# Performance work log

Hardware: AMD Instinct MI355X
Metric: run time of the kernel (lower is better)

## Reference

```python
import jax, jax.numpy as jnp
import numpy as np

LN_EPS = 1e-5


def setup_inputs() -> dict:
    key = jax.random.key(0)
    k1, k2, k3, k4 = jax.random.split(key, 4)
    b, n, d, o, m = 64, 196, 768, 196, 2
    return {
        "x": jax.random.normal(k1, (b, n, d), dtype=jnp.float32),
        "ln_w": jnp.ones((d,), dtype=jnp.float32),
        "ln_b": jnp.zeros((d,), dtype=jnp.float32),
        "sw": jax.random.normal(k2, (o, m, n), dtype=jnp.float32),
        "sb": jax.random.normal(k3, (o, m, n), dtype=jnp.float32),
        "dw": jax.random.normal(k4, (o, m), dtype=jnp.float32),
    }


def reference(x, ln_w, ln_b, sw, sb, dw):
    # LayerNorm over last dim (dim=768)
    mu = jnp.mean(x, axis=-1, keepdims=True)
    var = jnp.mean(jnp.square(x - mu), axis=-1, keepdims=True)
    y = (x - mu) * jax.lax.rsqrt(var + LN_EPS) * ln_w + ln_b  # (b, n, d)

    # Original: repeat y to (b,d,o,m,n), apply sw*y+sb, sum over n.
    # With no synapse activation / dropout this is exactly a contraction:
    # s[b,d,o,m] = sum_n sw[o,m,n]*y[b,n,d] + sum_n sb[o,m,n]
    s = jnp.einsum('bnd,omn->bdom', y, sw) + jnp.sum(sb, axis=-1)  # (b,d,o,m)

    # dendritic weighting then sum over branches m
    t = jnp.sum(dw * s, axis=-1)  # (b, d, o)

    # soma = nn.GELU (exact erf form)
    out = jax.nn.gelu(t, approximate=False)

    out = jnp.transpose(out, (0, 2, 1))  # (b, o, d) == (b, n, d)
    return x * (out + 1.0)
```

## Files before the change

kernel.cpp:

```cpp
#include <hip/hip_runtime.h>
#include <math.h>


#define B_   64
#define N_   196
#define D_   768
#define KQ   7
#define NKO  28
#define OPAD 256

typedef __attribute__((ext_vector_type(8))) short bf16x8;
typedef __attribute__((ext_vector_type(4))) float f32x4;

__device__ __forceinline__ unsigned short bf16_rne(float f) {
    unsigned u = __builtin_bit_cast(unsigned, f);
    u += 0x7FFFu + ((u >> 16) & 1u);
    return (unsigned short)(u >> 16);
}
__device__ __forceinline__ float bf16_to_f(unsigned short h) {
    unsigned u = ((unsigned)h) << 16;
    return __builtin_bit_cast(float, u);
}

__global__ void prep_w_kernel(const float* __restrict__ sw,
                              const float* __restrict__ sb,
                              const float* __restrict__ dw,
                              unsigned short* __restrict__ Wfh,
                              unsigned short* __restrict__ Wfl,
                              float* __restrict__ rowsum,
                              float* __restrict__ cvec) {
    int o = blockIdx.x;
    int t = threadIdx.x;
    float w0 = 0.f, w1 = 0.f;
    if (o < N_) { w0 = dw[o * 2 + 0]; w1 = dw[o * 2 + 1]; }
    float val = 0.f, sbp = 0.f;
    if (o < N_ && t < N_) {
        val = w0 * sw[(o * 2 + 0) * N_ + t] + w1 * sw[(o * 2 + 1) * N_ + t];
        sbp = w0 * sb[(o * 2 + 0) * N_ + t] + w1 * sb[(o * 2 + 1) * N_ + t];
    }
    if (t < KQ * 32) {
        unsigned short h = bf16_rne(val);
        int addr = ((o >> 4) * KQ + (t >> 5)) * 512
                 + (((t >> 3) & 3) * 16 + (o & 15)) * 8 + (t & 7);
        Wfh[addr] = h;
        Wfl[addr] = bf16_rne(val - bf16_to_f(h));
    }
    __shared__ float r1[256], r2[256];
    r1[t] = val; r2[t] = sbp;
    __syncthreads();
    for (int s = 128; s > 0; s >>= 1) {
        if (t < s) { r1[t] += r1[t + s]; r2[t] += r2[t + s]; }
        __syncthreads();
    }
    if (t == 0) { rowsum[o] = r1[0]; cvec[o] = r2[0]; }
}

__global__ __launch_bounds__(512) void ln_split_kernel(
    const float* __restrict__ x,
    const float* __restrict__ ln_w,
    unsigned short* __restrict__ Bh,
    unsigned short* __restrict__ Bl) {
    const int koct = blockIdx.x, b = blockIdx.y;
    const int t = threadIdx.x, w = t >> 6, lane = t & 63;
    const int k = koct * 8 + w;
    __shared__ float xs[8][768];

    float4 v0 = make_float4(0.f, 0.f, 0.f, 0.f);
    float4 v1 = v0, v2 = v0;
    if (k < N_) {
        const float4* xr = reinterpret_cast<const float4*>(x + ((size_t)b * N_ + k) * D_);
        v0 = xr[lane]; v1 = xr[lane + 64]; v2 = xr[lane + 128];
    }
    float s = v0.x + v0.y + v0.z + v0.w
            + v1.x + v1.y + v1.z + v1.w
            + v2.x + v2.y + v2.z + v2.w;
    float q = v0.x*v0.x + v0.y*v0.y + v0.z*v0.z + v0.w*v0.w
            + v1.x*v1.x + v1.y*v1.y + v1.z*v1.z + v1.w*v1.w
            + v2.x*v2.x + v2.y*v2.y + v2.z*v2.z + v2.w*v2.w;
    #pragma unroll
    for (int off = 32; off >= 1; off >>= 1) {
        s += __shfl_xor(s, off);
        q += __shfl_xor(q, off);
    }
    const float mu   = s * (1.0f / D_);
    const float var  = q * (1.0f / D_) - mu * mu;
    const float rstd = rsqrtf(var + 1e-5f);

    const float4* lw4 = reinterpret_cast<const float4*>(ln_w);
    float4 w0 = lw4[lane], w1 = lw4[lane + 64], w2 = lw4[lane + 128];
    float4 o0, o1, o2;
    o0.x = (v0.x - mu) * rstd * w0.x;  o0.y = (v0.y - mu) * rstd * w0.y;
    o0.z = (v0.z - mu) * rstd * w0.z;  o0.w = (v0.w - mu) * rstd * w0.w;
    o1.x = (v1.x - mu) * rstd * w1.x;  o1.y = (v1.y - mu) * rstd * w1.y;
    o1.z = (v1.z - mu) * rstd * w1.z;  o1.w = (v1.w - mu) * rstd * w1.w;
    o2.x = (v2.x - mu) * rstd * w2.x;  o2.y = (v2.y - mu) * rstd * w2.y;
    o2.z = (v2.z - mu) * rstd * w2.z;  o2.w = (v2.w - mu) * rstd * w2.w;
    *reinterpret_cast<float4*>(&xs[w][lane * 4])       = o0;
    *reinterpret_cast<float4*>(&xs[w][lane * 4 + 256]) = o1;
    *reinterpret_cast<float4*>(&xs[w][lane * 4 + 512]) = o2;
    __syncthreads();

    for (int d = t; d < D_; d += 512) {
        bf16x8 hv, lv;
        #pragma unroll
        for (int kk = 0; kk < 8; ++kk) {
            float v = xs[kk][d];
            unsigned short h = bf16_rne(v);
            hv[kk] = (short)h;
            lv[kk] = (short)bf16_rne(v - bf16_to_f(h));
        }
        const size_t base = (((size_t)b * NKO + koct) * D_ + d) * 8;
        *reinterpret_cast<bf16x8*>(Bh + base) = hv;
        *reinterpret_cast<bf16x8*>(Bl + base) = lv;
    }
}

__global__ __launch_bounds__(512, 2) void gemm_bpk_kernel(
    const float* __restrict__ x,
    const float* __restrict__ ln_b,
    const unsigned short* __restrict__ Wfh,
    const unsigned short* __restrict__ Wfl,
    const unsigned short* __restrict__ Bh,
    const unsigned short* __restrict__ Bl,
    const float* __restrict__ rowsum,
    const float* __restrict__ cvec,
    float* __restrict__ out) {
    const int b  = blockIdx.y;
    const int d0 = blockIdx.x * 48;
    const int t = threadIdx.x;
    const int w = t >> 6, lane = t & 63;
    const int m16 = lane & 15, g = lane >> 4;

    const float* xb = x + (size_t)b * (N_ * D_);

    f32x4 acc[2][3];
    #pragma unroll
    for (int i = 0; i < 2; ++i)
        #pragma unroll
        for (int j = 0; j < 3; ++j)
            acc[i][j] = (f32x4){0.f, 0.f, 0.f, 0.f};

    bf16x8 bhr[2][3], blr[2][3], ahr[2][2], alr[2][2];

    #define LOADB(s, c) do {                                                  \
        const size_t krow = ((size_t)b * NKO + (c) * 4 + g) * D_;             \
        _Pragma("unroll")                                                     \
        for (int nf = 0; nf < 3; ++nf) {                                      \
            const size_t e = (krow + d0 + nf * 16 + m16) * 8;                 \
            bhr[s][nf] = *reinterpret_cast<const bf16x8*>(Bh + e);            \
            blr[s][nf] = *reinterpret_cast<const bf16x8*>(Bl + e);            \
        } } while (0)

    #define LOADA(s, c) do {                                                  \
        _Pragma("unroll")                                                     \
        for (int mf = 0; mf < 2; ++mf) {                                      \
            const size_t ab = ((size_t)((w * 2 + mf) * KQ + (c))) * 512 + lane * 8; \
            ahr[s][mf] = *reinterpret_cast<const bf16x8*>(Wfh + ab);          \
            alr[s][mf] = *reinterpret_cast<const bf16x8*>(Wfl + ab);          \
        } } while (0)

    LOADB(0, 0);
    LOADA(0, 0);

    #pragma unroll
    for (int c = 0; c < KQ; ++c) {
        const int s = c & 1;
        if (c + 1 < KQ) {
            LOADB(s ^ 1, c + 1);
            LOADA(s ^ 1, c + 1);
        }
        #pragma unroll
        for (int nf = 0; nf < 3; ++nf) {
            #pragma unroll
            for (int mf = 0; mf < 2; ++mf) {
                acc[mf][nf] = __builtin_amdgcn_mfma_f32_16x16x32_bf16(ahr[s][mf], bhr[s][nf], acc[mf][nf], 0, 0, 0);
                acc[mf][nf] = __builtin_amdgcn_mfma_f32_16x16x32_bf16(ahr[s][mf], blr[s][nf], acc[mf][nf], 0, 0, 0);
                acc[mf][nf] = __builtin_amdgcn_mfma_f32_16x16x32_bf16(alr[s][mf], bhr[s][nf], acc[mf][nf], 0, 0, 0);
            }
        }
    }
    #undef LOADB
    #undef LOADA

    float lbv[3];
    #pragma unroll
    for (int nf = 0; nf < 3; ++nf) lbv[nf] = ln_b[d0 + nf * 16 + m16];
    #pragma unroll
    for (int mf = 0; mf < 2; ++mf) {
        const int obase = (w * 2 + mf) * 16 + g * 4;
        f32x4 rs4 = *reinterpret_cast<const f32x4*>(rowsum + obase);
        f32x4 cc4 = *reinterpret_cast<const f32x4*>(cvec + obase);
        float xres[4][3];
        #pragma unroll
        for (int r = 0; r < 4; ++r) {
            const int o = obase + r;
            #pragma unroll
            for (int nf = 0; nf < 3; ++nf)
                xres[r][nf] = (o < N_) ? xb[(size_t)o * D_ + d0 + nf * 16 + m16] : 0.f;
        }
        #pragma unroll
        for (int r = 0; r < 4; ++r) {
            const int o = obase + r;
            if (o < N_) {
                #pragma unroll
                for (int nf = 0; nf < 3; ++nf) {
                    const int d = d0 + nf * 16 + m16;
                    float T = acc[mf][nf][r] + fmaf(lbv[nf], rs4[r], cc4[r]);
                    float gl = 0.5f * T * (1.0f + erff(T * 0.70710678118654752f));
                    out[((size_t)(b * N_ + o)) * D_ + d] = xres[r][nf] * (gl + 1.0f);
                }
            }
        }
    }
}

extern "C" void kernel_launch(void* const* d_in, const int* in_sizes, int n_in,
                              void* d_out, int out_size, void* d_ws, size_t ws_size,
                              hipStream_t stream) {
    const float* x    = (const float*)d_in[0];
    const float* ln_w = (const float*)d_in[1];
    const float* ln_b = (const float*)d_in[2];
    const float* sw   = (const float*)d_in[3];
    const float* sb   = (const float*)d_in[4];
    const float* dw   = (const float*)d_in[5];
    float* out = (float*)d_out;

    float* wsf = (float*)d_ws;
    float* rowsum = wsf;
    float* cvec   = rowsum + OPAD;
    unsigned short* Wfh = (unsigned short*)(cvec + OPAD);
    unsigned short* Wfl = Wfh + OPAD * (KQ * 32);
    unsigned short* Bh  = Wfl + OPAD * (KQ * 32);
    unsigned short* Bl  = Bh + (size_t)B_ * NKO * D_ * 8;

    prep_w_kernel<<<OPAD, 256, 0, stream>>>(sw, sb, dw, Wfh, Wfl, rowsum, cvec);
    ln_split_kernel<<<dim3(NKO, B_), 512, 0, stream>>>(x, ln_w, Bh, Bl);
    gemm_bpk_kernel<<<dim3(16, B_), 512, 0, stream>>>(
        x, ln_b, Wfh, Wfl, Bh, Bl, rowsum, cvec, out);
}
```

Measured before the change: 56.15 us.

## Stage B operand in LDS via direct global-to-LDS loads, widen d tile to 64

```diff
diff --git a/kernel.cpp b/kernel.cpp
--- a/kernel.cpp
+++ b/kernel.cpp
@@ -20,6 +20,12 @@
 __device__ __forceinline__ float bf16_to_f(unsigned short h) {
     unsigned u = ((unsigned)h) << 16;
     return __builtin_bit_cast(float, u);
+}
+
+typedef __attribute__((address_space(3))) unsigned int lds_u32_t;
+typedef const __attribute__((address_space(1))) unsigned int glb_u32_t;
+__device__ __forceinline__ void gload_lds16(const void* g, void* l) {
+    __builtin_amdgcn_global_load_lds((glb_u32_t*)g, (lds_u32_t*)l, 16, 0, 0);
 }
 
 __global__ void prep_w_kernel(const float* __restrict__ sw,
@@ -115,7 +121,7 @@
     }
 }
 
-__global__ __launch_bounds__(512, 2) void gemm_bpk_kernel(
+__global__ __launch_bounds__(512, 4) void gemm_bpk_kernel(
     const float* __restrict__ x,
     const float* __restrict__ ln_b,
     const unsigned short* __restrict__ Wfh,
@@ -126,76 +132,84 @@
     const float* __restrict__ cvec,
     float* __restrict__ out) {
     const int b  = blockIdx.y;
-    const int d0 = blockIdx.x * 48;
+    const int d0 = blockIdx.x * 64;
     const int t = threadIdx.x;
     const int w = t >> 6, lane = t & 63;
     const int m16 = lane & 15, g = lane >> 4;
 
+    __shared__ __align__(16) unsigned short BsH[KQ][2048];
+    __shared__ __align__(16) unsigned short BsL[KQ][2048];
+
     const float* xb = x + (size_t)b * (N_ * D_);
 
-    f32x4 acc[2][3];
+    const int half = w >> 2;
+    const int cell = (w & 3) * 64 + lane;
+    const int skoct = cell >> 6, sd = cell & 63;
+    const unsigned short* sbase = (half ? Bl : Bh)
+        + (((size_t)b * NKO + skoct) * D_ + d0 + sd) * 8;
+
+    #pragma unroll
+    for (int c = 0; c < KQ; ++c) {
+        gload_lds16(sbase + (size_t)c * 4 * D_ * 8,
+                    (half ? &BsL[c][cell * 8] : &BsH[c][cell * 8]));
+    }
+
+    f32x4 acc[2][4];
     #pragma unroll
     for (int i = 0; i < 2; ++i)
         #pragma unroll
-        for (int j = 0; j < 3; ++j)
+        for (int j = 0; j < 4; ++j)
             acc[i][j] = (f32x4){0.f, 0.f, 0.f, 0.f};
 
-    bf16x8 bhr[2][3], blr[2][3], ahr[2][2], alr[2][2];
-
-    #define LOADB(s, c) do {                                                  \
-        const size_t krow = ((size_t)b * NKO + (c) * 4 + g) * D_;             \
-        _Pragma("unroll")                                                     \
-        for (int nf = 0; nf < 3; ++nf) {                                      \
-            const size_t e = (krow + d0 + nf * 16 + m16) * 8;                 \
-            bhr[s][nf] = *reinterpret_cast<const bf16x8*>(Bh + e);            \
-            blr[s][nf] = *reinterpret_cast<const bf16x8*>(Bl + e);            \
-        } } while (0)
-
-    #define LOADA(s, c) do {                                                  \
-        _Pragma("unroll")                                                     \
-        for (int mf = 0; mf < 2; ++mf) {                                      \
-            const size_t ab = ((size_t)((w * 2 + mf) * KQ + (c))) * 512 + lane * 8; \
-            ahr[s][mf] = *reinterpret_cast<const bf16x8*>(Wfh + ab);          \
-            alr[s][mf] = *reinterpret_cast<const bf16x8*>(Wfl + ab);          \
-        } } while (0)
-
-    LOADB(0, 0);
-    LOADA(0, 0);
+    bf16x8 ah[2][2], al[2][2];
+    #pragma unroll
+    for (int mf = 0; mf < 2; ++mf) {
+        const size_t ab = ((size_t)((w * 2 + mf) * KQ)) * 512 + lane * 8;
+        ah[0][mf] = *reinterpret_cast<const bf16x8*>(Wfh + ab);
+        al[0][mf] = *reinterpret_cast<const bf16x8*>(Wfl + ab);
+    }
+
+    __syncthreads();
 
     #pragma unroll
     for (int c = 0; c < KQ; ++c) {
         const int s = c & 1;
         if (c + 1 < KQ) {
-            LOADB(s ^ 1, c + 1);
-            LOADA(s ^ 1, c + 1);
-        }
-        #pragma unroll
-        for (int nf = 0; nf < 3; ++nf) {
             #pragma unroll
             for (int mf = 0; mf < 2; ++mf) {
-                acc[mf][nf] = __builtin_amdgcn_mfma_f32_16x16x32_bf16(ahr[s][mf], bhr[s][nf], acc[mf][nf], 0, 0, 0);
-                acc[mf][nf] = __builtin_amdgcn_mfma_f32_16x16x32_bf16(ahr[s][mf], blr[s][nf], acc[mf][nf], 0, 0, 0);
-                acc[mf][nf] = __builtin_amdgcn_mfma_f32_16x16x32_bf16(alr[s][mf], bhr[s][nf], acc[mf][nf], 0, 0, 0);
+                const size_t ab = ((size_t)((w * 2 + mf) * KQ + c + 1)) * 512 + lane * 8;
+                ah[s ^ 1][mf] = *reinterpret_cast<const bf16x8*>(Wfh + ab);
+                al[s ^ 1][mf] = *reinterpret_cast<const bf16x8*>(Wfl + ab);
             }
         }
-    }
-    #undef LOADB
-    #undef LOADA
-
-    float lbv[3];
-    #pragma unroll
-    for (int nf = 0; nf < 3; ++nf) lbv[nf] = ln_b[d0 + nf * 16 + m16];
+        #pragma unroll
+        for (int nf = 0; nf < 4; ++nf) {
+            const int ba = (g * 64 + nf * 16 + m16) * 8;
+            bf16x8 bh = *reinterpret_cast<const bf16x8*>(&BsH[c][ba]);
+            bf16x8 bl = *reinterpret_cast<const bf16x8*>(&BsL[c][ba]);
+            #pragma unroll
+            for (int mf = 0; mf < 2; ++mf) {
+                acc[mf][nf] = __builtin_amdgcn_mfma_f32_16x16x32_bf16(ah[s][mf], bh, acc[mf][nf], 0, 0, 0);
+                acc[mf][nf] = __builtin_amdgcn_mfma_f32_16x16x32_bf16(ah[s][mf], bl, acc[mf][nf], 0, 0, 0);
+                acc[mf][nf] = __builtin_amdgcn_mfma_f32_16x16x32_bf16(al[s][mf], bh, acc[mf][nf], 0, 0, 0);
+            }
+        }
+    }
+
+    float lbv[4];
+    #pragma unroll
+    for (int nf = 0; nf < 4; ++nf) lbv[nf] = ln_b[d0 + nf * 16 + m16];
     #pragma unroll
     for (int mf = 0; mf < 2; ++mf) {
         const int obase = (w * 2 + mf) * 16 + g * 4;
         f32x4 rs4 = *reinterpret_cast<const f32x4*>(rowsum + obase);
         f32x4 cc4 = *reinterpret_cast<const f32x4*>(cvec + obase);
-        float xres[4][3];
+        float xres[4][4];
         #pragma unroll
         for (int r = 0; r < 4; ++r) {
             const int o = obase + r;
             #pragma unroll
-            for (int nf = 0; nf < 3; ++nf)
+            for (int nf = 0; nf < 4; ++nf)
                 xres[r][nf] = (o < N_) ? xb[(size_t)o * D_ + d0 + nf * 16 + m16] : 0.f;
         }
         #pragma unroll
@@ -203,7 +217,7 @@
             const int o = obase + r;
             if (o < N_) {
                 #pragma unroll
-                for (int nf = 0; nf < 3; ++nf) {
+                for (int nf = 0; nf < 4; ++nf) {
                     const int d = d0 + nf * 16 + m16;
                     float T = acc[mf][nf][r] + fmaf(lbv[nf], rs4[r], cc4[r]);
                     float gl = 0.5f * T * (1.0f + erff(T * 0.70710678118654752f));
@@ -235,6 +249,6 @@
 
     prep_w_kernel<<<OPAD, 256, 0, stream>>>(sw, sb, dw, Wfh, Wfl, rowsum, cvec);
     ln_split_kernel<<<dim3(NKO, B_), 512, 0, stream>>>(x, ln_w, Bh, Bl);
-    gemm_bpk_kernel<<<dim3(16, B_), 512, 0, stream>>>(
+    gemm_bpk_kernel<<<dim3(12, B_), 512, 0, stream>>>(
         x, ln_b, Wfh, Wfl, Bh, Bl, rowsum, cvec, out);
 }
```

New measurement: 56.67 us. About the same (+0.9%).
